# Performance work log

Measured on AMD Instinct MI355X. Metric: run time of the kernel, lower is better.

Reference implementation:

```python
import jax, jax.numpy as jnp
import numpy as np

EPS = 1e-5  # BatchNorm eps


def cbr(x, W, g, b, m, v):
    # 1x1 Conv (no bias) + inference BatchNorm + ReLU
    # x: [B,Cin,H,W], W: [Cout,Cin]
    y = jnp.einsum('oc,bchw->bohw', W, x)
    inv = g / jnp.sqrt(v + EPS)            # [Cout]
    y = y * inv[None, :, None, None] + (b - m * inv)[None, :, None, None]
    return jax.nn.relu(y)


def setup_inputs() -> dict:
    key = jax.random.key(0)
    ks = jax.random.split(key, 32)
    B, C, R, H, W = 4, 2048, 512, 64, 64
    d = {"feature": jax.random.normal(ks[0], (B, C, H, W), jnp.float32)}
    idx = 1
    for name, (cin, cout) in [("r", (C, R)), ("q", (R, R)), ("k", (R, R)), ("v", (R, R)), ("u", (R, C))]:
        d[name + "_W"] = jax.random.normal(ks[idx], (cout, cin), jnp.float32) * 0.02
        d[name + "_g"] = jax.random.uniform(ks[idx + 1], (cout,), jnp.float32)
        d[name + "_b"] = jax.random.normal(ks[idx + 2], (cout,), jnp.float32) * 0.1
        d[name + "_m"] = jax.random.normal(ks[idx + 3], (cout,), jnp.float32) * 0.1
        d[name + "_v"] = jax.random.uniform(ks[idx + 4], (cout,), jnp.float32)
        idx += 5
    return d


def reference(feature, r_W, r_g, r_b, r_m, r_v,
              q_W, q_g, q_b, q_m, q_v,
              k_W, k_g, k_b, k_m, k_v,
              v_W, v_g, v_b, v_m, v_v,
              u_W, u_g, u_b, u_m, u_v):
    B, C, H, W = feature.shape
    f = cbr(feature, r_W, r_g, r_b, r_m, r_v)          # [B,R,H,W]
    R = f.shape[1]
    N = H * W
    q = cbr(f, q_W, q_g, q_b, q_m, q_v).reshape(B, R, N)
    k = cbr(f, k_W, k_g, k_b, k_m, k_v).reshape(B, R, N)
    v = cbr(f, v_W, v_g, v_b, v_m, v_v).reshape(B, R, N)
    # similarity map over all spatial positions: [B,N,N]
    attn = jax.nn.softmax(jnp.einsum('bcn,bcm->bnm', q, k), axis=-1)
    upd = jnp.einsum('bnm,bcm->bnc', attn, v)          # [B,N,R]
    upd = upd.reshape(B, H, W, R).transpose(0, 3, 1, 2)  # [B,R,H,W]
    return cbr(f + upd, u_W, u_g, u_b, u_m, u_v)       # [B,C,H,W]
```

## Files before the change

kernel.cpp:

```cpp
#include <hip/hip_runtime.h>

#define EPSV 1e-5f

typedef unsigned short u16;
typedef __attribute__((ext_vector_type(8))) _Float16 half8;
typedef __attribute__((ext_vector_type(4))) float floatx4;

__device__ __forceinline__ float h2f(u16 h) {
    return (float)__builtin_bit_cast(_Float16, h);
}
__device__ __forceinline__ u16 f2h(float f) {
    _Float16 h = (_Float16)f;
    return __builtin_bit_cast(u16, h);
}

template <int MODE, typename OUTT>
__global__ __launch_bounds__(256)
void gemm_nt(const u16* __restrict__ A, const u16* __restrict__ B,
             OUTT* __restrict__ C_,
             const float* __restrict__ inv_, const float* __restrict__ beta_,
             const u16* __restrict__ addf,
             int K, int ldA, int ldB, int ldC,
             long strideA, long strideB, long strideC)
{
    __shared__ u16 As[2][128 * 32];
    __shared__ u16 Bs[2][128 * 32];

    const int tid = threadIdx.x;
    const int w = tid >> 6;
    const int l = tid & 63;

    int bx = blockIdx.x, by = blockIdx.y, bz = blockIdx.z;
    {
        const int gx = gridDim.x, gy = gridDim.y;
        const int nwg = gx * gy * (int)gridDim.z;
        if ((nwg & 7) == 0) {
            const int lin = bx + gx * (by + gy * bz);
            const int swz = (lin & 7) * (nwg >> 3) + (lin >> 3);
            bx = swz % gx;
            const int t = swz / gx;
            by = t % gy;
            bz = t / gy;
        }
    }
    const int j0 = bx * 128;
    const int i0 = by * 128;

    const u16* Ab = A + (long)bz * strideA;
    const u16* Bb = B + (long)bz * strideB;

    const int srow = w * 16 + (l >> 2);
    const int skel = (l & 3) * 8;

    const int i_base = (w >> 1) * 64;
    const int j_base = (w & 1) * 64;
    const int lm = l & 15;
    const int kq = l >> 4;

    floatx4 acc[4][4];
    #pragma unroll
    for (int a = 0; a < 4; ++a)
        #pragma unroll
        for (int b = 0; b < 4; ++b) acc[a][b] = (floatx4)(0.0f);

    auto stage = [&](int buf, int k0) {
        const u16* ga0 = Ab + (long)(i0 + srow) * ldA + k0 + skel;
        const u16* ga1 = Ab + (long)(i0 + 64 + srow) * ldA + k0 + skel;
        const u16* gb0 = Bb + (long)(j0 + srow) * ldB + k0 + skel;
        const u16* gb1 = Bb + (long)(j0 + 64 + srow) * ldB + k0 + skel;
        char* la0 = (char*)&As[buf][0] + w * 1024;
        char* la1 = (char*)&As[buf][0] + 4096 + w * 1024;
        char* lb0 = (char*)&Bs[buf][0] + w * 1024;
        char* lb1 = (char*)&Bs[buf][0] + 4096 + w * 1024;
        __builtin_amdgcn_global_load_lds(
            (const __attribute__((address_space(1))) unsigned int*)(const void*)ga0,
            (__attribute__((address_space(3))) unsigned int*)(void*)la0, 16, 0, 0);
        __builtin_amdgcn_global_load_lds(
            (const __attribute__((address_space(1))) unsigned int*)(const void*)ga1,
            (__attribute__((address_space(3))) unsigned int*)(void*)la1, 16, 0, 0);
        __builtin_amdgcn_global_load_lds(
            (const __attribute__((address_space(1))) unsigned int*)(const void*)gb0,
            (__attribute__((address_space(3))) unsigned int*)(void*)lb0, 16, 0, 0);
        __builtin_amdgcn_global_load_lds(
            (const __attribute__((address_space(1))) unsigned int*)(const void*)gb1,
            (__attribute__((address_space(3))) unsigned int*)(void*)lb1, 16, 0, 0);
    };

    stage(0, 0);
    __syncthreads();

    int cur = 0;
    for (int k0 = 0; k0 < K; k0 += 32) {
        if (k0 + 32 < K) stage(cur ^ 1, k0 + 32);

        half8 af[4], bf[4];
        #pragma unroll
        for (int t = 0; t < 4; ++t) {
            af[t] = *(const half8*)&As[cur][(i_base + t * 16 + lm) * 32 + kq * 8];
            bf[t] = *(const half8*)&Bs[cur][(j_base + t * 16 + lm) * 32 + kq * 8];
        }
        #pragma unroll
        for (int ti = 0; ti < 4; ++ti)
            #pragma unroll
            for (int tj = 0; tj < 4; ++tj)
                acc[ti][tj] = __builtin_amdgcn_mfma_f32_16x16x32_f16(
                    af[ti], bf[tj], acc[ti][tj], 0, 0, 0);

        __syncthreads();
        cur ^= 1;
    }

    OUTT* Cb = C_ + (long)bz * strideC;
    const u16* addb = (MODE == 3) ? addf + (long)bz * strideC : nullptr;
    #pragma unroll
    for (int ti = 0; ti < 4; ++ti) {
        #pragma unroll
        for (int tj = 0; tj < 4; ++tj) {
            const int jj = j0 + j_base + tj * 16 + lm;
            float cinv = 0.f, cbeta = 0.f;
            if (MODE == 1) { cinv = inv_[jj]; cbeta = beta_[jj]; }
            #pragma unroll
            for (int r = 0; r < 4; ++r) {
                const int ii = i0 + i_base + ti * 16 + kq * 4 + r;
                float val = acc[ti][tj][r];
                if (MODE == 1) val = fmaxf(val * cinv + cbeta, 0.0f);
                if (MODE == 2) {
                    float iv = inv_[ii], bt = beta_[ii];
                    val = fmaxf(val * iv + bt, 0.0f);
                }
                if (MODE == 3) val += h2f(addb[(long)ii * ldC + jj]);
                if (sizeof(OUTT) == 4) {
                    ((float*)Cb)[(long)ii * ldC + jj] = val;
                } else {
                    ((u16*)Cb)[(long)ii * ldC + jj] = f2h(val);
                }
            }
        }
    }
}

__global__ __launch_bounds__(256)
void conv_weight(const float* __restrict__ W, const float* __restrict__ g,
                 const float* __restrict__ b, const float* __restrict__ m,
                 const float* __restrict__ v,
                 u16* __restrict__ Wb, float* __restrict__ inv_,
                 float* __restrict__ beta_, int cout, long n)
{
    for (long idx = (long)blockIdx.x * 256 + threadIdx.x; idx < n;
         idx += (long)gridDim.x * 256)
        Wb[idx] = f2h(W[idx]);
    int c = blockIdx.x * 256 + threadIdx.x;
    if (c < cout) {
        float iv = g[c] * rsqrtf(v[c] + EPSV);
        inv_[c] = iv;
        beta_[c] = b[c] - m[c] * iv;
    }
}

__global__ __launch_bounds__(256)
void transpose_conv(const float* __restrict__ in, u16* __restrict__ out,
                    int C, int N)
{
    __shared__ float t[32][33];
    const int n0 = blockIdx.x * 32, c0 = blockIdx.y * 32;
    const float* inb = in + (long)blockIdx.z * C * N;
    u16* outb = out + (long)blockIdx.z * C * N;
    const int tx = threadIdx.x & 31, ty = threadIdx.x >> 5;
    #pragma unroll
    for (int rr = 0; rr < 32; rr += 8)
        t[ty + rr][tx] = inb[(long)(c0 + ty + rr) * N + n0 + tx];
    __syncthreads();
    #pragma unroll
    for (int rr = 0; rr < 32; rr += 8)
        outb[(long)(n0 + ty + rr) * C + c0 + tx] = f2h(t[tx][ty + rr]);
}

__global__ __launch_bounds__(256)
void softmax_f16(const float* __restrict__ S, u16* __restrict__ P)
{
    __shared__ float buf[4096];
    __shared__ float red[256];
    const float* p = S + (long)blockIdx.y * 4096 * 4096 + (long)blockIdx.x * 4096;
    u16* o = P + (long)blockIdx.y * 4096 * 4096 + (long)blockIdx.x * 4096;
    const int tid = threadIdx.x;

    float lmax = -3.4e38f;
    for (int i = tid; i < 4096; i += 256) {
        float x = p[i];
        buf[i] = x;
        lmax = fmaxf(lmax, x);
    }
    red[tid] = lmax;
    __syncthreads();
    for (int s = 128; s > 0; s >>= 1) {
        if (tid < s) red[tid] = fmaxf(red[tid], red[tid + s]);
        __syncthreads();
    }
    const float mx = red[0];
    __syncthreads();

    float lsum = 0.0f;
    for (int i = tid; i < 4096; i += 256) {
        float e = __expf(buf[i] - mx);
        buf[i] = e;
        lsum += e;
    }
    red[tid] = lsum;
    __syncthreads();
    for (int s = 128; s > 0; s >>= 1) {
        if (tid < s) red[tid] += red[tid + s];
        __syncthreads();
    }
    const float invs = 1.0f / red[0];
    __syncthreads();

    for (int i = tid; i < 4096; i += 256) o[i] = f2h(buf[i] * invs);
}

extern "C" void kernel_launch(void* const* d_in, const int* in_sizes, int n_in,
                              void* d_out, int out_size, void* d_ws, size_t ws_size,
                              hipStream_t stream)
{
    (void)in_sizes; (void)n_in; (void)out_size; (void)ws_size;
    constexpr int B = 4, C = 2048, R = 512, N = 4096;
    constexpr long NR = (long)N * R;
    constexpr long NC = (long)N * C;
    constexpr long NN = (long)N * N;
    constexpr long NQK = (long)N * 1024;

    const float* feature = (const float*)d_in[0];
    const float* W_[5]  = {(const float*)d_in[1],  (const float*)d_in[6],
                           (const float*)d_in[11], (const float*)d_in[16],
                           (const float*)d_in[21]};
    const float* G_[5]  = {(const float*)d_in[2],  (const float*)d_in[7],
                           (const float*)d_in[12], (const float*)d_in[17],
                           (const float*)d_in[22]};
    const float* Bb_[5] = {(const float*)d_in[3],  (const float*)d_in[8],
                           (const float*)d_in[13], (const float*)d_in[18],
                           (const float*)d_in[23]};
    const float* M_[5]  = {(const float*)d_in[4],  (const float*)d_in[9],
                           (const float*)d_in[14], (const float*)d_in[19],
                           (const float*)d_in[24]};
    const float* V_[5]  = {(const float*)d_in[5],  (const float*)d_in[10],
                           (const float*)d_in[15], (const float*)d_in[20],
                           (const float*)d_in[25]};

    char* base = (char*)d_ws;
    size_t off = 0;
    float* S     = (float*)base;
    u16*   featT = (u16*)base;
    off += (size_t)B * NN * 4;
    u16* fT  = (u16*)(base + off);                     off += (size_t)B * NR * 2;
    u16* qkT = (u16*)(base + off);                     off += (size_t)B * NQK * 2;
    u16* vC  = (u16*)(base + off);                     off += (size_t)B * NR * 2;
    u16* gT  = (u16*)(base + off);                     off += (size_t)B * NN * 0 + (size_t)B * NR * 2;
    u16* Pc  = (u16*)(base + off);                     off += (size_t)B * NN * 2;
    u16* Wb_r  = (u16*)(base + off);  off += (size_t)R * C * 2;
    u16* WbQK  = (u16*)(base + off);  off += (size_t)1024 * R * 2;
    u16* Wb_v  = (u16*)(base + off);  off += (size_t)R * R * 2;
    u16* Wb_u  = (u16*)(base + off);  off += (size_t)C * R * 2;
    off = (off + 255) & ~(size_t)255;
    float* inv_r  = (float*)(base + off);  off += 8192;
    float* beta_r = (float*)(base + off);  off += 8192;
    float* invQK  = (float*)(base + off);  off += 8192;
    float* betaQK = (float*)(base + off);  off += 8192;
    float* inv_v  = (float*)(base + off);  off += 8192;
    float* beta_v = (float*)(base + off);  off += 8192;
    float* inv_u  = (float*)(base + off);  off += 8192;
    float* beta_u = (float*)(base + off);  off += 8192;

    float* out = (float*)d_out;
    const dim3 blk(256);

    conv_weight<<<512, blk, 0, stream>>>(W_[0], G_[0], Bb_[0], M_[0], V_[0],
                                         Wb_r, inv_r, beta_r, R, (long)R * C);
    conv_weight<<<512, blk, 0, stream>>>(W_[1], G_[1], Bb_[1], M_[1], V_[1],
                                         WbQK, invQK, betaQK, R, (long)R * R);
    conv_weight<<<512, blk, 0, stream>>>(W_[2], G_[2], Bb_[2], M_[2], V_[2],
                                         WbQK + (size_t)R * R, invQK + R, betaQK + R,
                                         R, (long)R * R);
    conv_weight<<<512, blk, 0, stream>>>(W_[3], G_[3], Bb_[3], M_[3], V_[3],
                                         Wb_v, inv_v, beta_v, R, (long)R * R);
    conv_weight<<<512, blk, 0, stream>>>(W_[4], G_[4], Bb_[4], M_[4], V_[4],
                                         Wb_u, inv_u, beta_u, C, (long)C * R);

    transpose_conv<<<dim3(N / 32, C / 32, B), blk, 0, stream>>>(feature, featT, C, N);

    gemm_nt<1, u16><<<dim3(R / 128, N / 128, B), blk, 0, stream>>>(
        featT, Wb_r, fT, inv_r, beta_r, nullptr,
        C, C, C, R, NC, 0, NR);

    gemm_nt<1, u16><<<dim3(1024 / 128, N / 128, B), blk, 0, stream>>>(
        fT, WbQK, qkT, invQK, betaQK, nullptr,
        R, R, R, 1024, NR, 0, NQK);

    gemm_nt<2, u16><<<dim3(N / 128, R / 128, B), blk, 0, stream>>>(
        Wb_v, fT, vC, inv_v, beta_v, nullptr,
        R, R, R, N, 0, NR, NR);

    gemm_nt<0, float><<<dim3(N / 128, N / 128, B), blk, 0, stream>>>(
        qkT, qkT + 512, S, nullptr, nullptr, nullptr,
        R, 1024, 1024, N, NQK, NQK, NN);

    softmax_f16<<<dim3(N, B), blk, 0, stream>>>(S, Pc);

    gemm_nt<3, u16><<<dim3(R / 128, N / 128, B), blk, 0, stream>>>(
        Pc, vC, gT, nullptr, nullptr, fT,
        N, N, N, R, NN, NR, NR);

    gemm_nt<2, float><<<dim3(N / 128, C / 128, B), blk, 0, stream>>>(
        Wb_u, gT, out, inv_u, beta_u, nullptr,
        R, R, R, N, 0, NR, NC);
}
```

Measured before the change: 793.6 us.

## Template GEMM tile sizes and split score/softmax per batch

Makes the GEMM tile shape a template parameter (TM x TN) with a generic staging loop. The R=512-sized GEMMs now use 128x64 or 64x128 tiles, which doubles the workgroup count to fill more CUs. The score GEMM and softmax now run per batch in a loop rather than as one batched launch. That per-batch split aims to keep each batch's fp32 score matrix hot in cache for the softmax read, at the cost of more kernel launches.

Measured after the change: 799.9 us. No clear change (+0.8%).

```diff
diff --git a/kernel.cpp b/kernel.cpp
--- a/kernel.cpp
+++ b/kernel.cpp
@@ -14,7 +14,7 @@
     return __builtin_bit_cast(u16, h);
 }
 
-template <int MODE, typename OUTT>
+template <int MODE, typename OUTT, int TM, int TN>
 __global__ __launch_bounds__(256)
 void gemm_nt(const u16* __restrict__ A, const u16* __restrict__ B,
              OUTT* __restrict__ C_,
@@ -23,8 +23,16 @@
              int K, int ldA, int ldB, int ldC,
              long strideA, long strideB, long strideC)
 {
-    __shared__ u16 As[2][128 * 32];
-    __shared__ u16 Bs[2][128 * 32];
+    static_assert(TM % 64 == 0 && TN % 64 == 0, "tile multiple of 64");
+    constexpr int AISS = TM / 16;
+    constexpr int BISS = TN / 16;
+    constexpr int NISS = AISS + BISS;
+    constexpr int WISS = NISS / 4;
+    constexpr int RM = TM / 32;
+    constexpr int RN = TN / 32;
+
+    __shared__ u16 As[2][TM * 32];
+    __shared__ u16 Bs[2][TN * 32];
 
     const int tid = threadIdx.x;
     const int w = tid >> 6;
@@ -43,69 +51,69 @@
             bz = t / gy;
         }
     }
-    const int j0 = bx * 128;
-    const int i0 = by * 128;
+    const int j0 = bx * TN;
+    const int i0 = by * TM;
 
     const u16* Ab = A + (long)bz * strideA;
     const u16* Bb = B + (long)bz * strideB;
 
-    const int srow = w * 16 + (l >> 2);
+    const int srow = l >> 2;
     const int skel = (l & 3) * 8;
 
-    const int i_base = (w >> 1) * 64;
-    const int j_base = (w & 1) * 64;
+    const int i_base = (w >> 1) * (TM / 2);
+    const int j_base = (w & 1) * (TN / 2);
     const int lm = l & 15;
     const int kq = l >> 4;
 
-    floatx4 acc[4][4];
+    floatx4 acc[RM][RN];
     #pragma unroll
-    for (int a = 0; a < 4; ++a)
-        #pragma unroll
-        for (int b = 0; b < 4; ++b) acc[a][b] = (floatx4)(0.0f);
+    for (int a = 0; a < RM; ++a)
+        #pragma unroll
+        for (int b = 0; b < RN; ++b) acc[a][b] = (floatx4)(0.0f);
 
     auto stage = [&](int buf, int k0) {
-        const u16* ga0 = Ab + (long)(i0 + srow) * ldA + k0 + skel;
-        const u16* ga1 = Ab + (long)(i0 + 64 + srow) * ldA + k0 + skel;
-        const u16* gb0 = Bb + (long)(j0 + srow) * ldB + k0 + skel;
-        const u16* gb1 = Bb + (long)(j0 + 64 + srow) * ldB + k0 + skel;
-        char* la0 = (char*)&As[buf][0] + w * 1024;
-        char* la1 = (char*)&As[buf][0] + 4096 + w * 1024;
-        char* lb0 = (char*)&Bs[buf][0] + w * 1024;
-        char* lb1 = (char*)&Bs[buf][0] + 4096 + w * 1024;
-        __builtin_amdgcn_global_load_lds(
-            (const __attribute__((address_space(1))) unsigned int*)(const void*)ga0,
-            (__attribute__((address_space(3))) unsigned int*)(void*)la0, 16, 0, 0);
-        __builtin_amdgcn_global_load_lds(
-            (const __attribute__((address_space(1))) unsigned int*)(const void*)ga1,
-            (__attribute__((address_space(3))) unsigned int*)(void*)la1, 16, 0, 0);
-        __builtin_amdgcn_global_load_lds(
-            (const __attribute__((address_space(1))) unsigned int*)(const void*)gb0,
-            (__attribute__((address_space(3))) unsigned int*)(void*)lb0, 16, 0, 0);
-        __builtin_amdgcn_global_load_lds(
-            (const __attribute__((address_space(1))) unsigned int*)(const void*)gb1,
-            (__attribute__((address_space(3))) unsigned int*)(void*)lb1, 16, 0, 0);
+        #pragma unroll
+        for (int s = 0; s < WISS; ++s) {
+            const int q = w + 4 * s;
+            const u16* gsrc;
+            char* ldst;
+            if (q < AISS) {
+                gsrc = Ab + (long)(i0 + q * 16 + srow) * ldA + k0 + skel;
+                ldst = (char*)&As[buf][0] + q * 1024;
+            } else {
+                const int qb = q - AISS;
+                gsrc = Bb + (long)(j0 + qb * 16 + srow) * ldB + k0 + skel;
+                ldst = (char*)&Bs[buf][0] + qb * 1024;
+            }
+            __builtin_amdgcn_global_load_lds(
+                (const __attribute__((address_space(1))) unsigned int*)(const void*)gsrc,
+                (__attribute__((address_space(3))) unsigned int*)(void*)ldst,
+                16, 0, 0);
+        }
     };
 
+    const int nt = K >> 5;
     stage(0, 0);
     __syncthreads();
-
     int cur = 0;
-    for (int k0 = 0; k0 < K; k0 += 32) {
-        if (k0 + 32 < K) stage(cur ^ 1, k0 + 32);
-
-        half8 af[4], bf[4];
-        #pragma unroll
-        for (int t = 0; t < 4; ++t) {
-            af[t] = *(const half8*)&As[cur][(i_base + t * 16 + lm) * 32 + kq * 8];
-            bf[t] = *(const half8*)&Bs[cur][(j_base + t * 16 + lm) * 32 + kq * 8];
-        }
-        #pragma unroll
-        for (int ti = 0; ti < 4; ++ti)
+    for (int t = 0; t < nt; ++t) {
+        if (t + 1 < nt) stage(cur ^ 1, (t + 1) << 5);
+
+        const u16* Ac = &As[cur][0];
+        const u16* Bc = &Bs[cur][0];
+        half8 af[RM], bf[RN];
+        #pragma unroll
+        for (int ti = 0; ti < RM; ++ti)
+            af[ti] = *(const half8*)&Ac[(i_base + ti * 16 + lm) * 32 + kq * 8];
+        #pragma unroll
+        for (int tj = 0; tj < RN; ++tj)
+            bf[tj] = *(const half8*)&Bc[(j_base + tj * 16 + lm) * 32 + kq * 8];
+        #pragma unroll
+        for (int ti = 0; ti < RM; ++ti)
             #pragma unroll
-            for (int tj = 0; tj < 4; ++tj)
+            for (int tj = 0; tj < RN; ++tj)
                 acc[ti][tj] = __builtin_amdgcn_mfma_f32_16x16x32_f16(
                     af[ti], bf[tj], acc[ti][tj], 0, 0, 0);
-
         __syncthreads();
         cur ^= 1;
     }
@@ -113,9 +121,9 @@
     OUTT* Cb = C_ + (long)bz * strideC;
     const u16* addb = (MODE == 3) ? addf + (long)bz * strideC : nullptr;
     #pragma unroll
-    for (int ti = 0; ti < 4; ++ti) {
-        #pragma unroll
-        for (int tj = 0; tj < 4; ++tj) {
+    for (int ti = 0; ti < RM; ++ti) {
+        #pragma unroll
+        for (int tj = 0; tj < RN; ++tj) {
             const int jj = j0 + j_base + tj * 16 + lm;
             float cinv = 0.f, cbeta = 0.f;
             if (MODE == 1) { cinv = inv_[jj]; cbeta = beta_[jj]; }
@@ -180,8 +188,8 @@
 {
     __shared__ float buf[4096];
     __shared__ float red[256];
-    const float* p = S + (long)blockIdx.y * 4096 * 4096 + (long)blockIdx.x * 4096;
-    u16* o = P + (long)blockIdx.y * 4096 * 4096 + (long)blockIdx.x * 4096;
+    const float* p = S + (long)blockIdx.x * 4096;
+    u16* o = P + (long)blockIdx.x * 4096;
     const int tid = threadIdx.x;
 
     float lmax = -3.4e38f;
@@ -253,7 +261,7 @@
     u16* fT  = (u16*)(base + off);                     off += (size_t)B * NR * 2;
     u16* qkT = (u16*)(base + off);                     off += (size_t)B * NQK * 2;
     u16* vC  = (u16*)(base + off);                     off += (size_t)B * NR * 2;
-    u16* gT  = (u16*)(base + off);                     off += (size_t)B * NN * 0 + (size_t)B * NR * 2;
+    u16* gT  = (u16*)(base + off);                     off += (size_t)B * NR * 2;
     u16* Pc  = (u16*)(base + off);                     off += (size_t)B * NN * 2;
     u16* Wb_r  = (u16*)(base + off);  off += (size_t)R * C * 2;
     u16* WbQK  = (u16*)(base + off);  off += (size_t)1024 * R * 2;
@@ -286,29 +294,32 @@
 
     transpose_conv<<<dim3(N / 32, C / 32, B), blk, 0, stream>>>(feature, featT, C, N);
 
-    gemm_nt<1, u16><<<dim3(R / 128, N / 128, B), blk, 0, stream>>>(
+    gemm_nt<1, u16, 128, 64><<<dim3(R / 64, N / 128, B), blk, 0, stream>>>(
         featT, Wb_r, fT, inv_r, beta_r, nullptr,
         C, C, C, R, NC, 0, NR);
 
-    gemm_nt<1, u16><<<dim3(1024 / 128, N / 128, B), blk, 0, stream>>>(
+    gemm_nt<1, u16, 128, 128><<<dim3(1024 / 128, N / 128, B), blk, 0, stream>>>(
         fT, WbQK, qkT, invQK, betaQK, nullptr,
         R, R, R, 1024, NR, 0, NQK);
 
-    gemm_nt<2, u16><<<dim3(N / 128, R / 128, B), blk, 0, stream>>>(
+    gemm_nt<2, u16, 64, 128><<<dim3(N / 128, R / 64, B), blk, 0, stream>>>(
         Wb_v, fT, vC, inv_v, beta_v, nullptr,
         R, R, R, N, 0, NR, NR);
 
-    gemm_nt<0, float><<<dim3(N / 128, N / 128, B), blk, 0, stream>>>(
-        qkT, qkT + 512, S, nullptr, nullptr, nullptr,
-        R, 1024, 1024, N, NQK, NQK, NN);
-
-    softmax_f16<<<dim3(N, B), blk, 0, stream>>>(S, Pc);
-
-    gemm_nt<3, u16><<<dim3(R / 128, N / 128, B), blk, 0, stream>>>(
+    for (int b = 0; b < B; ++b) {
+        gemm_nt<0, float, 128, 128><<<dim3(N / 128, N / 128, 1), blk, 0, stream>>>(
+            qkT + (long)b * NQK, qkT + (long)b * NQK + 512, S + (long)b * NN,
+            nullptr, nullptr, nullptr,
+            R, 1024, 1024, N, 0, 0, 0);
+        softmax_f16<<<dim3(N), blk, 0, stream>>>(S + (long)b * NN,
+                                                 Pc + (long)b * NN);
+    }
+
+    gemm_nt<3, u16, 128, 64><<<dim3(R / 64, N / 128, B), blk, 0, stream>>>(
         Pc, vC, gT, nullptr, nullptr, fT,
         N, N, N, R, NN, NR, NR);
 
-    gemm_nt<2, float><<<dim3(N / 128, C / 128, B), blk, 0, stream>>>(
+    gemm_nt<2, float, 128, 128><<<dim3(N / 128, C / 128, B), blk, 0, stream>>>(
         Wb_u, gT, out, inv_u, beta_u, nullptr,
         R, R, R, N, 0, NR, NC);
 }
```

## Split-K the reduce and PV GEMMs and interleave per-batch QK/softmax

Applied to the files above, without the earlier changes.

Adds a two-way split-K mode to the GEMM kernel, used for the first 1x1 conv (flattened over batch) and the attention-times-V GEMM, with a new combine kernel that sums the partials and applies BN+ReLU or the residual add. The goal is more workgroups for these low-tile-count GEMMs, which otherwise underfill the GPU. The QK GEMM and softmax are now launched per batch so each score slab is likely still in cache when softmax reads it. In exchange there are extra fp32 partial writes and reads, extra launches, and a hardcoded 160MB workspace offset for the partial buffer.

Measured after the change: 815.3 us. 2.7% more time.

```diff
diff --git a/kernel.cpp b/kernel.cpp
--- a/kernel.cpp
+++ b/kernel.cpp
@@ -5,6 +5,7 @@
 typedef unsigned short u16;
 typedef __attribute__((ext_vector_type(8))) _Float16 half8;
 typedef __attribute__((ext_vector_type(4))) float floatx4;
+typedef __attribute__((ext_vector_type(4))) unsigned short ushort4v;
 
 __device__ __forceinline__ float h2f(u16 h) {
     return (float)__builtin_bit_cast(_Float16, h);
@@ -21,7 +22,8 @@
              const float* __restrict__ inv_, const float* __restrict__ beta_,
              const u16* __restrict__ addf,
              int K, int ldA, int ldB, int ldC,
-             long strideA, long strideB, long strideC)
+             long strideA, long strideB, long strideC,
+             long strideS, int nsplit)
 {
     __shared__ u16 As[2][128 * 32];
     __shared__ u16 Bs[2][128 * 32];
@@ -43,11 +45,17 @@
             bz = t / gy;
         }
     }
+    int ks = 0;
+    if (nsplit == 2) {
+        const int gxh = (int)gridDim.x >> 1;
+        if (bx >= gxh) { ks = 1; bx -= gxh; }
+    }
     const int j0 = bx * 128;
     const int i0 = by * 128;
-
-    const u16* Ab = A + (long)bz * strideA;
-    const u16* Bb = B + (long)bz * strideB;
+    const long koff = (long)ks * K;
+
+    const u16* Ab = A + (long)bz * strideA + koff;
+    const u16* Bb = B + (long)bz * strideB + koff;
 
     const int srow = w * 16 + (l >> 2);
     const int skel = (l & 3) * 8;
@@ -86,18 +94,20 @@
             (__attribute__((address_space(3))) unsigned int*)(void*)lb1, 16, 0, 0);
     };
 
+    const int nt = K >> 5;
     stage(0, 0);
     __syncthreads();
-
     int cur = 0;
-    for (int k0 = 0; k0 < K; k0 += 32) {
-        if (k0 + 32 < K) stage(cur ^ 1, k0 + 32);
-
+    for (int t = 0; t < nt; ++t) {
+        if (t + 1 < nt) stage(cur ^ 1, (t + 1) << 5);
+
+        const u16* Ac = &As[cur][0];
+        const u16* Bc = &Bs[cur][0];
         half8 af[4], bf[4];
         #pragma unroll
-        for (int t = 0; t < 4; ++t) {
-            af[t] = *(const half8*)&As[cur][(i_base + t * 16 + lm) * 32 + kq * 8];
-            bf[t] = *(const half8*)&Bs[cur][(j_base + t * 16 + lm) * 32 + kq * 8];
+        for (int tt = 0; tt < 4; ++tt) {
+            af[tt] = *(const half8*)&Ac[(i_base + tt * 16 + lm) * 32 + kq * 8];
+            bf[tt] = *(const half8*)&Bc[(j_base + tt * 16 + lm) * 32 + kq * 8];
         }
         #pragma unroll
         for (int ti = 0; ti < 4; ++ti)
@@ -105,12 +115,11 @@
             for (int tj = 0; tj < 4; ++tj)
                 acc[ti][tj] = __builtin_amdgcn_mfma_f32_16x16x32_f16(
                     af[ti], bf[tj], acc[ti][tj], 0, 0, 0);
-
         __syncthreads();
         cur ^= 1;
     }
 
-    OUTT* Cb = C_ + (long)bz * strideC;
+    OUTT* Cb = C_ + (long)bz * strideC + (long)ks * strideS;
     const u16* addb = (MODE == 3) ? addf + (long)bz * strideC : nullptr;
     #pragma unroll
     for (int ti = 0; ti < 4; ++ti) {
@@ -139,6 +148,31 @@
     }
 }
 
+template <int MODE>
+__global__ __launch_bounds__(256)
+void combine2(const float* __restrict__ P, const u16* __restrict__ addf,
+              const float* __restrict__ inv_, const float* __restrict__ beta_,
+              u16* __restrict__ outp, long n4, long s4, int J)
+{
+    for (long i = (long)blockIdx.x * 256 + threadIdx.x; i < n4;
+         i += (long)gridDim.x * 256) {
+        floatx4 a = ((const floatx4*)P)[i];
+        floatx4 b = ((const floatx4*)P)[i + s4];
+        ushort4v o;
+        const int j0 = (int)((i * 4) & (J - 1));
+        ushort4v ad;
+        if (MODE == 3) ad = *(const ushort4v*)&addf[i * 4];
+        #pragma unroll
+        for (int r = 0; r < 4; ++r) {
+            float v = a[r] + b[r];
+            if (MODE == 1) v = fmaxf(v * inv_[j0 + r] + beta_[j0 + r], 0.0f);
+            if (MODE == 3) v += h2f(ad[r]);
+            o[r] = f2h(v);
+        }
+        *(ushort4v*)&outp[i * 4] = o;
+    }
+}
+
 __global__ __launch_bounds__(256)
 void conv_weight(const float* __restrict__ W, const float* __restrict__ g,
                  const float* __restrict__ b, const float* __restrict__ m,
@@ -180,8 +214,8 @@
 {
     __shared__ float buf[4096];
     __shared__ float red[256];
-    const float* p = S + (long)blockIdx.y * 4096 * 4096 + (long)blockIdx.x * 4096;
-    u16* o = P + (long)blockIdx.y * 4096 * 4096 + (long)blockIdx.x * 4096;
+    const float* p = S + (long)blockIdx.x * 4096;
+    u16* o = P + (long)blockIdx.x * 4096;
     const int tid = threadIdx.x;
 
     float lmax = -3.4e38f;
@@ -227,6 +261,7 @@
     constexpr long NC = (long)N * C;
     constexpr long NN = (long)N * N;
     constexpr long NQK = (long)N * 1024;
+    constexpr long TOT = (long)B * NR;
 
     const float* feature = (const float*)d_in[0];
     const float* W_[5]  = {(const float*)d_in[1],  (const float*)d_in[6],
@@ -249,11 +284,12 @@
     size_t off = 0;
     float* S     = (float*)base;
     u16*   featT = (u16*)base;
+    float* Psplit = (float*)(base + (size_t)160 * 1024 * 1024);
     off += (size_t)B * NN * 4;
     u16* fT  = (u16*)(base + off);                     off += (size_t)B * NR * 2;
     u16* qkT = (u16*)(base + off);                     off += (size_t)B * NQK * 2;
     u16* vC  = (u16*)(base + off);                     off += (size_t)B * NR * 2;
-    u16* gT  = (u16*)(base + off);                     off += (size_t)B * NN * 0 + (size_t)B * NR * 2;
+    u16* gT  = (u16*)(base + off);                     off += (size_t)B * NR * 2;
     u16* Pc  = (u16*)(base + off);                     off += (size_t)B * NN * 2;
     u16* Wb_r  = (u16*)(base + off);  off += (size_t)R * C * 2;
     u16* WbQK  = (u16*)(base + off);  off += (size_t)1024 * R * 2;
@@ -286,29 +322,36 @@
 
     transpose_conv<<<dim3(N / 32, C / 32, B), blk, 0, stream>>>(feature, featT, C, N);
 
-    gemm_nt<1, u16><<<dim3(R / 128, N / 128, B), blk, 0, stream>>>(
-        featT, Wb_r, fT, inv_r, beta_r, nullptr,
-        C, C, C, R, NC, 0, NR);
+    gemm_nt<0, float><<<dim3(2 * R / 128, (B * N) / 128, 1), blk, 0, stream>>>(
+        featT, Wb_r, Psplit, nullptr, nullptr, nullptr,
+        1024, C, C, R, 0, 0, 0, TOT, 2);
+    combine2<1><<<2048, blk, 0, stream>>>(Psplit, nullptr, inv_r, beta_r,
+                                          fT, TOT / 4, TOT / 4, R);
 
     gemm_nt<1, u16><<<dim3(1024 / 128, N / 128, B), blk, 0, stream>>>(
         fT, WbQK, qkT, invQK, betaQK, nullptr,
-        R, R, R, 1024, NR, 0, NQK);
+        R, R, R, 1024, NR, 0, NQK, 0, 1);
 
     gemm_nt<2, u16><<<dim3(N / 128, R / 128, B), blk, 0, stream>>>(
         Wb_v, fT, vC, inv_v, beta_v, nullptr,
-        R, R, R, N, 0, NR, NR);
-
-    gemm_nt<0, float><<<dim3(N / 128, N / 128, B), blk, 0, stream>>>(
-        qkT, qkT + 512, S, nullptr, nullptr, nullptr,
-        R, 1024, 1024, N, NQK, NQK, NN);
-
-    softmax_f16<<<dim3(N, B), blk, 0, stream>>>(S, Pc);
-
-    gemm_nt<3, u16><<<dim3(R / 128, N / 128, B), blk, 0, stream>>>(
-        Pc, vC, gT, nullptr, nullptr, fT,
-        N, N, N, R, NN, NR, NR);
+        R, R, R, N, 0, NR, NR, 0, 1);
+
+    for (int b = 0; b < B; ++b) {
+        gemm_nt<0, float><<<dim3(N / 128, N / 128, 1), blk, 0, stream>>>(
+            qkT + (long)b * NQK, qkT + (long)b * NQK + 512, S + (long)b * NN,
+            nullptr, nullptr, nullptr,
+            R, 1024, 1024, N, 0, 0, 0, 0, 1);
+        softmax_f16<<<dim3(N), blk, 0, stream>>>(S + (long)b * NN,
+                                                 Pc + (long)b * NN);
+    }
+
+    gemm_nt<0, float><<<dim3(2 * R / 128, N / 128, B), blk, 0, stream>>>(
+        Pc, vC, Psplit, nullptr, nullptr, nullptr,
+        2048, N, N, R, NN, NR, NR, TOT, 2);
+    combine2<3><<<2048, blk, 0, stream>>>(Psplit, fT, nullptr, nullptr,
+                                          gT, TOT / 4, TOT / 4, R);
 
     gemm_nt<2, float><<<dim3(N / 128, C / 128, B), blk, 0, stream>>>(
         Wb_u, gT, out, inv_u, beta_u, nullptr,
-        R, R, R, N, 0, NR, NC);
-}
+        R, R, R, N, 0, NR, NC, 0, 1);
+}
```
